# Kernel tuning notes

Hardware: AMD Instinct MI355X
Metric: run time of the kernel (lower is better)

## Reference

```python
import jax, jax.numpy as jnp
import numpy as np

B, L, KD, ED, H = 8, 4096, 512, 1024, 8  # batch, seq, key_dim, embed_dim, n_heads
LN_EPS = 1e-5


def setup_inputs() -> dict:
    key = jax.random.key(0)
    ks = jax.random.split(key, 6)
    keys = jax.random.normal(ks[0], (B, L, KD), dtype=jnp.float32)
    values = jax.random.normal(ks[1], (B, L, ED), dtype=jnp.float32)
    # learned params
    query = jax.random.normal(ks[2], (H, 1, KD // H), dtype=jnp.float32) * 0.02
    k_bias = jax.random.normal(ks[3], (KD,), dtype=jnp.float32) / np.sqrt(KD).astype(np.float32)
    v_bias = jnp.zeros((ED,), dtype=jnp.float32)
    softmax_weight = 1.0 + 0.01 * jax.random.normal(ks[4], (H, 1, L + 1), dtype=jnp.float32)
    softmax_bias = 0.01 * jax.random.normal(ks[5], (H, 1, L + 1), dtype=jnp.float32)
    gamma = jnp.ones((ED,), dtype=jnp.float32)
    beta = jnp.zeros((ED,), dtype=jnp.float32)
    return {"keys": keys, "values": values, "query": query, "k_bias": k_bias,
            "v_bias": v_bias, "softmax_weight": softmax_weight,
            "softmax_bias": softmax_bias, "gamma": gamma, "beta": beta}


def reference(keys, values, query, k_bias, v_bias, softmax_weight, softmax_bias, gamma, beta):
    b = keys.shape[0]
    # append learned bias token to keys and values  -> [B, L+1, *]
    keys = jnp.concatenate([keys, jnp.broadcast_to(k_bias, (b, 1, k_bias.shape[0]))], axis=1)
    values = jnp.concatenate([values, jnp.broadcast_to(v_bias, (b, 1, v_bias.shape[0]))], axis=1)
    lp = keys.shape[1]
    # torch multihead_reshape is a raw contiguous view [B,L,C] -> [B*H, L, C/H]
    K = keys.reshape(b * H, lp, keys.shape[2] // H)      # [B*H, L+1, KD/H]
    V = values.reshape(b * H, lp, values.shape[2] // H)  # [B*H, L+1, ED/H]
    Q = jnp.tile(query, (b, 1, 1))                       # [B*H, 1, KD/H]
    scores = jnp.einsum('bqd,bld->bql', Q, K)            # [B*H, 1, L+1]
    scores = scores * jnp.tile(softmax_weight, (b, 1, 1)) + jnp.tile(softmax_bias, (b, 1, 1))
    attn = jax.nn.softmax(scores, axis=-1)               # [B*H, 1, L+1]
    A = jnp.einsum('bql,bld->bqd', attn, V)              # [B*H, 1, ED/H]
    A = A.reshape(b, 1, -1)                              # multihead_unshape -> [B, 1, ED]
    # LayerNorm over embed dim (torch default eps=1e-5, biased var)
    mean = jnp.mean(A, axis=-1, keepdims=True)
    var = jnp.var(A, axis=-1, keepdims=True)
    return (A - mean) * jax.lax.rsqrt(var + LN_EPS) * gamma + beta
```

## Files before the change

kernel.cpp:

```cpp
#include <hip/hip_runtime.h>

#define BATCH 8
#define LSEQ  4096
#define LP    4097
#define KDIM  512
#define EDIM  1024
#define NH    8
#define DK    64
#define DV    128
#define NG    64
#define SSTR  4112
#define NCK   32
#define RCK   129
#define NC    32
#define RC    129
#define LN_EPS 1e-5f

typedef float floatx4 __attribute__((ext_vector_type(4)));

__global__ __launch_bounds__(256) void lqa_scores_kernel(
    const float* __restrict__ keys, const float* __restrict__ k_bias,
    const float* __restrict__ query, const float* __restrict__ sw,
    const float* __restrict__ sb, float* __restrict__ p,
    float2* __restrict__ stats)
{
    const int chunk = blockIdx.x;
    const int g = blockIdx.y;
    const int b = g >> 3, h = g & 7;
    const int t = threadIdx.x;
    const int lane16 = t & 15;
    const int d0 = lane16 * 4;

    const floatx4 q = *reinterpret_cast<const floatx4*>(query + h * DK + d0);
    const float* kp = keys + (long long)b * (LSEQ * KDIM);
    const int fhead = h * (LP * DK);
    const int row0 = chunk * RCK;
    const int row_end = min(LP, row0 + RCK);
    float* prow = p + (long long)g * SSTR;
    const float* w = sw + h * LP;
    const float* bb = sb + h * LP;

    float mloc = -1e30f, zloc = 0.f;
    for (int row = row0 + (t >> 4); row < row_end; row += 16) {
        const int f = fhead + row * DK + d0;
        const floatx4 k = (f < LSEQ * KDIM)
            ? *reinterpret_cast<const floatx4*>(kp + f)
            : *reinterpret_cast<const floatx4*>(k_bias + (f - LSEQ * KDIM));
        float s = q.x * k.x + q.y * k.y + q.z * k.z + q.w * k.w;
        s += __shfl_xor(s, 1);
        s += __shfl_xor(s, 2);
        s += __shfl_xor(s, 4);
        s += __shfl_xor(s, 8);
        if (lane16 == 0) {
            const float tv = s * w[row] + bb[row];
            prow[row] = tv;
            if (tv > mloc) { zloc = zloc * __expf(mloc - tv) + 1.f; mloc = tv; }
            else            zloc += __expf(tv - mloc);
        }
    }

    __shared__ float mred[256], zred[256];
    mred[t] = mloc; zred[t] = zloc;
    for (int off = 128; off > 0; off >>= 1) {
        __syncthreads();
        if (t < off) {
            const float m1 = mred[t], z1 = zred[t];
            const float m2 = mred[t + off], z2 = zred[t + off];
            const float m = fmaxf(m1, m2);
            mred[t] = m;
            zred[t] = z1 * __expf(m1 - m) + z2 * __expf(m2 - m);
        }
    }
    if (t == 0) stats[g * NCK + chunk] = make_float2(mred[0], zred[0]);
}

__global__ __launch_bounds__(256) void lqa_av_kernel(
    const float* __restrict__ values, const float* __restrict__ v_bias,
    const float* __restrict__ p, const float2* __restrict__ stats,
    float* __restrict__ partials)
{
    const int chunk = blockIdx.x;
    const int g = blockIdx.y;
    const int b = g >> 3, h = g & 7;
    const int t = threadIdx.x;
    const int srow = t >> 5;
    const int d0 = (t & 31) * 4;

    float m = -1e30f, Z = 0.f;
#pragma unroll
    for (int c = 0; c < NCK; ++c) {
        const float2 s = stats[g * NCK + c];
        const float mn = fmaxf(m, s.x);
        Z = Z * __expf(m - mn) + s.y * __expf(s.x - mn);
        m = mn;
    }
    const float rinv = 1.f / Z;

    const float* vp = values + (long long)b * (LSEQ * EDIM);
    const int fhead = h * (LP * DV);
    const float* prow = p + (long long)g * SSTR;
    const int row0 = chunk * RC;
    const int nrows = min(LP, row0 + RC) - row0;

    __shared__ float pw[RC];
    for (int r = t; r < nrows; r += 256)
        pw[r] = __expf(prow[row0 + r] - m) * rinv;
    __syncthreads();

    float acc[4] = {0.f, 0.f, 0.f, 0.f};
    for (int r = srow; r < nrows; r += 8) {
        const float wgt = pw[r];
        const int f = fhead + (row0 + r) * DV + d0;
        const floatx4 v = (f < LSEQ * EDIM)
            ? *reinterpret_cast<const floatx4*>(vp + f)
            : *reinterpret_cast<const floatx4*>(v_bias + (f - LSEQ * EDIM));
        acc[0] += wgt * v.x; acc[1] += wgt * v.y;
        acc[2] += wgt * v.z; acc[3] += wgt * v.w;
    }

    __shared__ float red[256 * 4];
#pragma unroll
    for (int j = 0; j < 4; ++j) red[t * 4 + j] = acc[j];
    for (int off = 128; off >= 32; off >>= 1) {
        __syncthreads();
        if (t < off) {
#pragma unroll
            for (int j = 0; j < 4; ++j) red[t * 4 + j] += red[(t + off) * 4 + j];
        }
    }
    __syncthreads();
    if (t < 32) {
        float* dst = partials + ((long long)(g * NC + chunk)) * DV + t * 4;
#pragma unroll
        for (int j = 0; j < 4; ++j) dst[j] = red[t * 4 + j];
    }
}

__global__ __launch_bounds__(256) void lqa_ln_kernel(
    const float* __restrict__ partials, const float* __restrict__ gamma,
    const float* __restrict__ beta, float* __restrict__ out)
{
    const int b = blockIdx.x;
    const int t = threadIdx.x;
    __shared__ float r1[256], r2[256];

    float a[4];
    float s1 = 0.f, s2 = 0.f;
#pragma unroll
    for (int i = 0; i < 4; ++i) {
        const int e = t + i * 256;
        const int h = e >> 7, d = e & 127;
        const float* src = partials + ((long long)((b * NH + h) * NC)) * DV + d;
        float sum = 0.f;
#pragma unroll
        for (int c = 0; c < NC; ++c) sum += src[c * DV];
        a[i] = sum;
        s1 += sum;
        s2 += sum * sum;
    }
    r1[t] = s1; r2[t] = s2; __syncthreads();
    for (int off = 128; off > 0; off >>= 1) {
        if (t < off) { r1[t] += r1[t + off]; r2[t] += r2[t + off]; }
        __syncthreads();
    }
    const float mean = r1[0] * (1.0f / EDIM);
    const float var = r2[0] * (1.0f / EDIM) - mean * mean;
    const float inv = rsqrtf(var + LN_EPS);
#pragma unroll
    for (int i = 0; i < 4; ++i) {
        const int e = t + i * 256;
        out[(long long)b * EDIM + e] = (a[i] - mean) * inv * gamma[e] + beta[e];
    }
}

extern "C" void kernel_launch(void* const* d_in, const int* in_sizes, int n_in,
                              void* d_out, int out_size, void* d_ws, size_t ws_size,
                              hipStream_t stream) {
    const float* keys   = (const float*)d_in[0];
    const float* values = (const float*)d_in[1];
    const float* query  = (const float*)d_in[2];
    const float* k_bias = (const float*)d_in[3];
    const float* v_bias = (const float*)d_in[4];
    const float* sw     = (const float*)d_in[5];
    const float* sb     = (const float*)d_in[6];
    const float* gamma  = (const float*)d_in[7];
    const float* beta   = (const float*)d_in[8];
    float* out = (float*)d_out;

    float* ws = (float*)d_ws;
    float* p = ws;
    float2* stats = (float2*)(ws + (long long)NG * SSTR);
    float* partials = ws + (long long)NG * SSTR + NG * NCK * 2;

    lqa_scores_kernel<<<dim3(NCK, NG), 256, 0, stream>>>(keys, k_bias, query, sw, sb, p, stats);
    lqa_av_kernel    <<<dim3(NC, NG),  256, 0, stream>>>(values, v_bias, p, stats, partials);
    lqa_ln_kernel    <<<BATCH,         256, 0, stream>>>(partials, gamma, beta, out);
}
```

Measured before the change: 264.6 us.

## Fuse score and AV passes with per-chunk softmax rescaled in combine kernel

Merges the scores kernel and the attention-times-values kernel into one kernel. Each block computes its chunk's scores into shared memory, applies a chunk-local softmax, accumulates its weighted V partial sums, and writes the chunk max and sum. The LayerNorm kernel now rescales each chunk's partials by its global softmax weight before summing. This drops one launch and the global round trip for scores, but each block now does the key reads and value reads back to back and has a few more barriers.

```diff
diff --git a/kernel.cpp b/kernel.cpp
--- a/kernel.cpp
+++ b/kernel.cpp
@@ -9,19 +9,17 @@
 #define DK    64
 #define DV    128
 #define NG    64
-#define SSTR  4112
-#define NCK   32
-#define RCK   129
 #define NC    32
 #define RC    129
 #define LN_EPS 1e-5f
 
 typedef float floatx4 __attribute__((ext_vector_type(4)));
 
-__global__ __launch_bounds__(256) void lqa_scores_kernel(
+__global__ __launch_bounds__(256) void lqa_fused_kernel(
     const float* __restrict__ keys, const float* __restrict__ k_bias,
+    const float* __restrict__ values, const float* __restrict__ v_bias,
     const float* __restrict__ query, const float* __restrict__ sw,
-    const float* __restrict__ sb, float* __restrict__ p,
+    const float* __restrict__ sb, float* __restrict__ partials,
     float2* __restrict__ stats)
 {
     const int chunk = blockIdx.x;
@@ -29,20 +27,25 @@
     const int b = g >> 3, h = g & 7;
     const int t = threadIdx.x;
     const int lane16 = t & 15;
-    const int d0 = lane16 * 4;
-
-    const floatx4 q = *reinterpret_cast<const floatx4*>(query + h * DK + d0);
+    const int d0k = lane16 * 4;
+
+    const int row0 = chunk * RC;
+    const int nrows = min(LP, row0 + RC) - row0;
+
+    __shared__ float ts[RC];
+    __shared__ float red1[256];
+    __shared__ float red4[256 * 4];
+
+    const floatx4 q = *reinterpret_cast<const floatx4*>(query + h * DK + d0k);
     const float* kp = keys + (long long)b * (LSEQ * KDIM);
-    const int fhead = h * (LP * DK);
-    const int row0 = chunk * RCK;
-    const int row_end = min(LP, row0 + RCK);
-    float* prow = p + (long long)g * SSTR;
+    const int fheadk = h * (LP * DK);
     const float* w = sw + h * LP;
     const float* bb = sb + h * LP;
 
-    float mloc = -1e30f, zloc = 0.f;
-    for (int row = row0 + (t >> 4); row < row_end; row += 16) {
-        const int f = fhead + row * DK + d0;
+    float mloc = -1e30f;
+    for (int r = (t >> 4); r < nrows; r += 16) {
+        const int row = row0 + r;
+        const int f = fheadk + row * DK + d0k;
         const floatx4 k = (f < LSEQ * KDIM)
             ? *reinterpret_cast<const floatx4*>(kp + f)
             : *reinterpret_cast<const floatx4*>(k_bias + (f - LSEQ * KDIM));
@@ -53,64 +56,42 @@
         s += __shfl_xor(s, 8);
         if (lane16 == 0) {
             const float tv = s * w[row] + bb[row];
-            prow[row] = tv;
-            if (tv > mloc) { zloc = zloc * __expf(mloc - tv) + 1.f; mloc = tv; }
-            else            zloc += __expf(tv - mloc);
+            ts[r] = tv;
+            mloc = fmaxf(mloc, tv);
         }
     }
-
-    __shared__ float mred[256], zred[256];
-    mred[t] = mloc; zred[t] = zloc;
+    red1[t] = mloc;
     for (int off = 128; off > 0; off >>= 1) {
         __syncthreads();
-        if (t < off) {
-            const float m1 = mred[t], z1 = zred[t];
-            const float m2 = mred[t + off], z2 = zred[t + off];
-            const float m = fmaxf(m1, m2);
-            mred[t] = m;
-            zred[t] = z1 * __expf(m1 - m) + z2 * __expf(m2 - m);
-        }
-    }
-    if (t == 0) stats[g * NCK + chunk] = make_float2(mred[0], zred[0]);
-}
-
-__global__ __launch_bounds__(256) void lqa_av_kernel(
-    const float* __restrict__ values, const float* __restrict__ v_bias,
-    const float* __restrict__ p, const float2* __restrict__ stats,
-    float* __restrict__ partials)
-{
-    const int chunk = blockIdx.x;
-    const int g = blockIdx.y;
-    const int b = g >> 3, h = g & 7;
-    const int t = threadIdx.x;
+        if (t < off) red1[t] = fmaxf(red1[t], red1[t + off]);
+    }
+    __syncthreads();
+    const float mc = red1[0];
+    __syncthreads();
+
+    float zloc = 0.f;
+    for (int r = t; r < nrows; r += 256) {
+        const float e = __expf(ts[r] - mc);
+        ts[r] = e;
+        zloc += e;
+    }
+    red1[t] = zloc;
+    for (int off = 128; off > 0; off >>= 1) {
+        __syncthreads();
+        if (t < off) red1[t] += red1[t + off];
+    }
+    __syncthreads();
+    const float zc = red1[0];
+
     const int srow = t >> 5;
-    const int d0 = (t & 31) * 4;
-
-    float m = -1e30f, Z = 0.f;
-#pragma unroll
-    for (int c = 0; c < NCK; ++c) {
-        const float2 s = stats[g * NCK + c];
-        const float mn = fmaxf(m, s.x);
-        Z = Z * __expf(m - mn) + s.y * __expf(s.x - mn);
-        m = mn;
-    }
-    const float rinv = 1.f / Z;
-
+    const int d0v = (t & 31) * 4;
     const float* vp = values + (long long)b * (LSEQ * EDIM);
-    const int fhead = h * (LP * DV);
-    const float* prow = p + (long long)g * SSTR;
-    const int row0 = chunk * RC;
-    const int nrows = min(LP, row0 + RC) - row0;
-
-    __shared__ float pw[RC];
-    for (int r = t; r < nrows; r += 256)
-        pw[r] = __expf(prow[row0 + r] - m) * rinv;
-    __syncthreads();
+    const int fheadv = h * (LP * DV);
 
     float acc[4] = {0.f, 0.f, 0.f, 0.f};
     for (int r = srow; r < nrows; r += 8) {
-        const float wgt = pw[r];
-        const int f = fhead + (row0 + r) * DV + d0;
+        const float wgt = ts[r];
+        const int f = fheadv + (row0 + r) * DV + d0v;
         const floatx4 v = (f < LSEQ * EDIM)
             ? *reinterpret_cast<const floatx4*>(vp + f)
             : *reinterpret_cast<const floatx4*>(v_bias + (f - LSEQ * EDIM));
@@ -118,31 +99,54 @@
         acc[2] += wgt * v.z; acc[3] += wgt * v.w;
     }
 
-    __shared__ float red[256 * 4];
-#pragma unroll
-    for (int j = 0; j < 4; ++j) red[t * 4 + j] = acc[j];
+#pragma unroll
+    for (int j = 0; j < 4; ++j) red4[t * 4 + j] = acc[j];
     for (int off = 128; off >= 32; off >>= 1) {
         __syncthreads();
         if (t < off) {
 #pragma unroll
-            for (int j = 0; j < 4; ++j) red[t * 4 + j] += red[(t + off) * 4 + j];
+            for (int j = 0; j < 4; ++j) red4[t * 4 + j] += red4[(t + off) * 4 + j];
         }
     }
     __syncthreads();
     if (t < 32) {
         float* dst = partials + ((long long)(g * NC + chunk)) * DV + t * 4;
 #pragma unroll
-        for (int j = 0; j < 4; ++j) dst[j] = red[t * 4 + j];
-    }
+        for (int j = 0; j < 4; ++j) dst[j] = red4[t * 4 + j];
+    }
+    if (t == 0) stats[g * NC + chunk] = make_float2(mc, zc);
 }
 
-__global__ __launch_bounds__(256) void lqa_ln_kernel(
-    const float* __restrict__ partials, const float* __restrict__ gamma,
-    const float* __restrict__ beta, float* __restrict__ out)
+__global__ __launch_bounds__(256) void lqa_combine_ln_kernel(
+    const float* __restrict__ partials, const float2* __restrict__ stats,
+    const float* __restrict__ gamma, const float* __restrict__ beta,
+    float* __restrict__ out)
 {
     const int b = blockIdx.x;
     const int t = threadIdx.x;
+    __shared__ float mh[NH], zh[NH];
+    __shared__ float wc[NH * NC];
     __shared__ float r1[256], r2[256];
+
+    if (t < NH) {
+        const float2* st = stats + (b * NH + t) * NC;
+        float m = -1e30f, Z = 0.f;
+#pragma unroll
+        for (int c = 0; c < NC; ++c) {
+            const float2 s = st[c];
+            const float mn = fmaxf(m, s.x);
+            Z = Z * __expf(m - mn) + s.y * __expf(s.x - mn);
+            m = mn;
+        }
+        mh[t] = m; zh[t] = Z;
+    }
+    __syncthreads();
+    {
+        const int h = t >> 5, c = t & 31;
+        const float2 s = stats[(b * NH + h) * NC + c];
+        wc[t] = __expf(s.x - mh[h]) / zh[h];
+    }
+    __syncthreads();
 
     float a[4];
     float s1 = 0.f, s2 = 0.f;
@@ -151,9 +155,10 @@
         const int e = t + i * 256;
         const int h = e >> 7, d = e & 127;
         const float* src = partials + ((long long)((b * NH + h) * NC)) * DV + d;
+        const float* wr = wc + h * NC;
         float sum = 0.f;
 #pragma unroll
-        for (int c = 0; c < NC; ++c) sum += src[c * DV];
+        for (int c = 0; c < NC; ++c) sum += src[c * DV] * wr[c];
         a[i] = sum;
         s1 += sum;
         s2 += sum * sum;
@@ -188,11 +193,11 @@
     float* out = (float*)d_out;
 
     float* ws = (float*)d_ws;
-    float* p = ws;
-    float2* stats = (float2*)(ws + (long long)NG * SSTR);
-    float* partials = ws + (long long)NG * SSTR + NG * NCK * 2;
-
-    lqa_scores_kernel<<<dim3(NCK, NG), 256, 0, stream>>>(keys, k_bias, query, sw, sb, p, stats);
-    lqa_av_kernel    <<<dim3(NC, NG),  256, 0, stream>>>(values, v_bias, p, stats, partials);
-    lqa_ln_kernel    <<<BATCH,         256, 0, stream>>>(partials, gamma, beta, out);
+    float* partials = ws;
+    float2* stats = (float2*)(ws + (long long)NG * NC * DV);
+
+    lqa_fused_kernel<<<dim3(NC, NG), 256, 0, stream>>>(
+        keys, k_bias, values, v_bias, query, sw, sb, partials, stats);
+    lqa_combine_ln_kernel<<<BATCH, 256, 0, stream>>>(
+        partials, stats, gamma, beta, out);
 }
```

New measurement: 258.4 us. -2.3%, faster.
